# Optimization experiments

Measured on AMD Instinct MI355X. Metric: run time of the kernel, lower is better.

Reference implementation:

```python
import jax, jax.numpy as jnp
import numpy as np

ALPHAS = [2.0 ** k for k in range(-3, 2)]  # cfg.model.mmd.alphas = 2.0
EPS = 1e-12


def _center(x):
    return x - x.mean(axis=-1, keepdims=True)


def _l2norm(x):
    return x / jnp.sqrt(jnp.sum(x * x, axis=-1, keepdims=True) + EPS)


def _multi_gauss(d2):
    # sum_a exp(-a * d2), fused over the alpha list
    out = jnp.exp(-ALPHAS[0] * d2)
    for a in ALPHAS[1:]:
        out = out + jnp.exp(-a * d2)
    return out


def _sq_dists_self(x):
    # x: [..., n, c] -> squared euclidean pairwise [..., n, n]
    sq = jnp.sum(x * x, axis=-1)  # [..., n]
    gram = jnp.einsum('...ic,...jc->...ij', x, x)
    d2 = sq[..., :, None] + sq[..., None, :] - 2.0 * gram
    return jnp.maximum(d2, 0.0)


def setup_inputs() -> dict:
    key = jax.random.key(0)
    k1, k2 = jax.random.split(key)
    support_xf = jax.random.normal(k1, (16, 5, 130, 640), dtype=jnp.float32)
    query_xf = jax.random.normal(k2, (16, 75, 25, 640), dtype=jnp.float32)
    return {"support_xf": support_xf, "query_xf": query_xf}


def reference(support_xf, query_xf):
    # support_xf: [b, n_way, ns, c], query_xf: [b, q, nq, c]
    b, n_way, ns, c = support_xf.shape
    _, q, nq, _ = query_xf.shape

    # centering over feature dim, then l2 norm (cfg.model.mmd.l2norm = True)
    s = _l2norm(_center(support_xf))
    t = _l2norm(_center(query_xf))

    # self Gram kernels
    k_ss = _multi_gauss(_sq_dists_self(s))  # [b, n_way, ns, ns]
    k_qq = _multi_gauss(_sq_dists_self(t))  # [b, q, nq, nq]

    # cross kernel: broadcast instead of materializing expanded 5D copies
    sn = jnp.sum(s * s, axis=-1)  # [b, n_way, ns]
    tn = jnp.sum(t * t, axis=-1)  # [b, q, nq]
    gram_qs = jnp.einsum('bwsc,bqtc->bqwst', s, t)  # [b, q, n_way, ns, nq]
    d2_qs = jnp.maximum(
        sn[:, None, :, :, None] + tn[:, :, None, None, :] - 2.0 * gram_qs, 0.0)
    k_qs = _multi_gauss(d2_qs)

    # MMD terms: unbiased self terms drop the diagonal
    mmd_s = (jnp.sum(k_ss, axis=(-1, -2)) - jnp.trace(k_ss, axis1=-2, axis2=-1)) \
        / (ns * (ns - 1))  # [b, n_way]
    mmd_q = (jnp.sum(k_qq, axis=(-1, -2)) - jnp.trace(k_qq, axis1=-2, axis2=-1)) \
        / (nq * (nq - 1))  # [b, q]
    mmd_qs = jnp.sum(k_qs, axis=(-1, -2)) / (ns * nq)  # [b, q, n_way]

    mmd_dis = mmd_s[:, None, :] + mmd_q[:, :, None] - 2.0 * mmd_qs  # [b, q, n_way]
    return mmd_dis
```

## Files before the change

### kernel.cpp

```cpp
#include <hip/hip_runtime.h>
#include <math.h>


#define EXP_C (-0.25f * 1.44269504088896340736f)

typedef __attribute__((ext_vector_type(8))) short bf16x8_t;
typedef __attribute__((ext_vector_type(4))) float f32x4_t;
typedef unsigned short u16;

#define GLOAD_LDS16(g, l)                                 \
  __builtin_amdgcn_global_load_lds(                       \
      (const __attribute__((address_space(1))) void*)(g), \
      (__attribute__((address_space(3))) void*)(l), 16, 0, 0)

__device__ __forceinline__ u16 f2bf(float f) {
  unsigned int u = __float_as_uint(f);
  unsigned int r = (u + 0x7fffu + ((u >> 16) & 1u)) >> 16;
  return (u16)r;
}

__device__ __forceinline__ float mgauss(float g) {
  float h = fmaxf(1.f - g, 0.f);
  float e1 = exp2f(h * EXP_C);
  float e2 = e1 * e1, e4 = e2 * e2, e8 = e4 * e4, e16 = e8 * e8;
  return e1 + e2 + e4 + e8 + e16;
}

__device__ __forceinline__ float wred(float v) {
#pragma unroll
  for (int m = 1; m < 64; m <<= 1) v += __shfl_xor(v, m, 64);
  return v;
}

__global__ void prep_kernel(const float* __restrict__ S,
                            const float* __restrict__ Q,
                            u16* __restrict__ SHL, u16* __restrict__ QHL,
                            float* __restrict__ accz) {
  int bid = blockIdx.x, tid = threadIdx.x;
  if (bid < 29) {
    int z = bid * 256 + tid;
    if (z < 7280) accz[z] = 0.f;
  }
  int wid = (bid << 2) | (tid >> 6);
  int lane = tid & 63;
  const float* src;
  u16* dst;
  if (wid < 10400) {
    src = S + (size_t)wid * 640;
    dst = SHL + (size_t)wid * 640;
  } else {
    int w2 = wid - 10400;
    src = Q + (size_t)w2 * 640;
    dst = QHL + (size_t)w2 * 640;
  }
  const float4* s4 = (const float4*)src;
  float4 a = s4[lane];
  float4 b = s4[lane + 64];
  float4 c = make_float4(0.f, 0.f, 0.f, 0.f);
  if (lane < 32) c = s4[lane + 128];
  float s = a.x + a.y + a.z + a.w + b.x + b.y + b.z + b.w + c.x + c.y + c.z +
            c.w;
  float ss = a.x * a.x + a.y * a.y + a.z * a.z + a.w * a.w + b.x * b.x +
             b.y * b.y + b.z * b.z + b.w * b.w + c.x * c.x + c.y * c.y +
             c.z * c.z + c.w * c.w;
#pragma unroll
  for (int m = 1; m < 64; m <<= 1) {
    s += __shfl_xor(s, m, 64);
    ss += __shfl_xor(ss, m, 64);
  }
  float mean = s * (1.f / 640.f);
  float inv = 1.f / sqrtf(fmaxf(ss - s * s * (1.f / 640.f), 0.f) + 1e-12f);
  ushort4* d4 = (ushort4*)dst;
  d4[lane] = make_ushort4(f2bf((a.x - mean) * inv), f2bf((a.y - mean) * inv),
                          f2bf((a.z - mean) * inv), f2bf((a.w - mean) * inv));
  d4[lane + 64] =
      make_ushort4(f2bf((b.x - mean) * inv), f2bf((b.y - mean) * inv),
                   f2bf((b.z - mean) * inv), f2bf((b.w - mean) * inv));
  if (lane < 32)
    d4[lane + 128] =
        make_ushort4(f2bf((c.x - mean) * inv), f2bf((c.y - mean) * inv),
                     f2bf((c.z - mean) * inv), f2bf((c.w - mean) * inv));
}

__global__ __launch_bounds__(256, 4) void grams_kernel(
    const u16* __restrict__ SHL, const u16* __restrict__ QHL,
    float* __restrict__ accS, float* __restrict__ accQ,
    float* __restrict__ accQS) {
  __shared__ __align__(16) u16 sA[128 * 64];
  __shared__ __align__(16) u16 sB[128 * 64];
  const int bid = blockIdx.x;
  const int id = (bid & 7) * 242 + (bid >> 3);
  const int tid = threadIdx.x;
  const int w = tid >> 6, l = tid & 63;

  int mode, gb, i0, j0, nx, ny;
  const u16 *pX, *pY;
  if (id < 1440) {
    mode = 0;
    gb = id / 90;
    int r = id % 90;
    i0 = (r % 6) * 128;
    j0 = (r / 6) * 128;
    pX = SHL + (size_t)gb * 650 * 640;
    pY = QHL + (size_t)gb * 1875 * 640;
    nx = 650;
    ny = 1875;
  } else if (id < 1696) {
    mode = 1;
    int t = id - 1440;
    gb = t >> 4;
    int p = t & 15;
    int ti, tj;
    if (p < 4) {
      ti = p >> 1;
      tj = p & 1;
    } else {
      int q = (p - 4) / 3, r3 = (p - 4) % 3;
      ti = (r3 == 0) ? q + 1 : q + 2;
      tj = (r3 == 1) ? q + 1 : q + 2;
    }
    i0 = ti * 128;
    j0 = tj * 128;
    pX = pY = SHL + (size_t)gb * 650 * 640;
    nx = ny = 650;
  } else {
    mode = 2;
    gb = id - 1696;
    i0 = 0;
    j0 = 0;
    pX = pY = QHL + (size_t)gb * 125 * 640;
    nx = ny = 125;
  }

  int st_r[4], st_c[4];
#pragma unroll
  for (int i = 0; i < 4; ++i) {
    int s = (w * 4 + i) * 64 + l;
    st_r[i] = s >> 3;
    st_c[i] = ((s & 7) ^ (st_r[i] & 7)) * 8;
  }

  f32x4_t av[4][4];
#pragma unroll
  for (int i = 0; i < 4; ++i)
#pragma unroll
    for (int j = 0; j < 4; ++j)
#pragma unroll
      for (int r = 0; r < 4; ++r) av[i][j][r] = 0.f;

  const int wr = w >> 1, wc = w & 1;
  const int R0 = wr * 64, C0 = wc * 64;
  const int lr = l & 15, lk8 = (l >> 4) * 8;

  for (int c = 0; c < 10; ++c) {
    int kb = c * 64;
#pragma unroll
    for (int i = 0; i < 4; ++i) {
      int vi = i0 + st_r[i];
      vi = vi < nx ? vi : nx - 1;
      GLOAD_LDS16(pX + (size_t)vi * 640 + kb + st_c[i], &sA[(w * 4 + i) * 512]);
      int vj = j0 + st_r[i];
      vj = vj < ny ? vj : ny - 1;
      GLOAD_LDS16(pY + (size_t)vj * 640 + kb + st_c[i], &sB[(w * 4 + i) * 512]);
    }
    __syncthreads();
#pragma unroll
    for (int ks = 0; ks < 2; ++ks) {
      bf16x8_t af[4], bfv[4];
      int kk = ks * 32 + lk8;
#pragma unroll
      for (int t = 0; t < 4; ++t) {
        int rr = R0 + t * 16 + lr;
        af[t] = *(const bf16x8_t*)&sA[rr * 64 + (kk ^ ((rr & 7) << 3))];
        int cc = C0 + t * 16 + lr;
        bfv[t] = *(const bf16x8_t*)&sB[cc * 64 + (kk ^ ((cc & 7) << 3))];
      }
#pragma unroll
      for (int i = 0; i < 4; ++i)
#pragma unroll
        for (int j = 0; j < 4; ++j)
          av[i][j] = __builtin_amdgcn_mfma_f32_16x16x32_bf16(af[i], bfv[j],
                                                             av[i][j], 0, 0, 0);
    }
    __syncthreads();
  }

  int gcv[4];
  bool cvv[4];
#pragma unroll
  for (int j = 0; j < 4; ++j) {
    gcv[j] = j0 + C0 + j * 16 + lr;
    cvv[j] = gcv[j] < ny;
  }

  if (mode == 0) {
    const int cbi = (i0 + R0) / 130;
    const int cbj = (j0 + C0) / 25;
    int cjr[4];
#pragma unroll
    for (int j = 0; j < 4; ++j) cjr[j] = gcv[j] / 25 - cbj;
    float ce[2][4] = {{0.f, 0.f, 0.f, 0.f}, {0.f, 0.f, 0.f, 0.f}};
#pragma unroll
    for (int i = 0; i < 4; ++i)
#pragma unroll
      for (int rr = 0; rr < 4; ++rr) {
        int gr = i0 + R0 + i * 16 + (l >> 4) * 4 + rr;
        bool rv = gr < 650;
        bool ra = (gr / 130) == cbi;
#pragma unroll
        for (int j = 0; j < 4; ++j) {
          float kv = mgauss(av[i][j][rr]);
          kv = (rv && cvv[j]) ? kv : 0.f;
          float k0 = ra ? kv : 0.f;
          ce[0][j] += k0;
          ce[1][j] += kv - k0;
        }
      }
#pragma unroll
    for (int a = 0; a < 2; ++a)
#pragma unroll
      for (int bq = 0; bq < 4; ++bq) {
        float t = 0.f;
#pragma unroll
        for (int j = 0; j < 4; ++j) t += (cjr[j] == bq) ? ce[a][j] : 0.f;
        t = wred(t);
        if (l == 0) {
          int ci = cbi + a, cj = cbj + bq;
          if (ci < 5 && cj < 75) atomicAdd(&accQS[gb * 375 + cj * 5 + ci], t);
        }
      }
  } else if (mode == 1) {
    const int cbi = (i0 + R0) / 130;
    int ccv[4];
#pragma unroll
    for (int j = 0; j < 4; ++j) ccv[j] = gcv[j] / 130;
    float ce[2][4] = {{0.f, 0.f, 0.f, 0.f}, {0.f, 0.f, 0.f, 0.f}};
#pragma unroll
    for (int i = 0; i < 4; ++i)
#pragma unroll
      for (int rr = 0; rr < 4; ++rr) {
        int gr = i0 + R0 + i * 16 + (l >> 4) * 4 + rr;
        bool rv = gr < 650;
        int rc = gr / 130;
        bool ra = rc == cbi;
#pragma unroll
        for (int j = 0; j < 4; ++j) {
          float kv = mgauss(av[i][j][rr]);
          bool val = rv && cvv[j] && (ccv[j] == rc) && (gr != gcv[j]);
          kv = val ? kv : 0.f;
          float k0 = ra ? kv : 0.f;
          ce[0][j] += k0;
          ce[1][j] += kv - k0;
        }
      }
#pragma unroll
    for (int a = 0; a < 2; ++a) {
      float t = wred(ce[a][0] + ce[a][1] + ce[a][2] + ce[a][3]);
      if (l == 0) {
        int ci = cbi + a;
        if (ci < 5) atomicAdd(&accS[gb * 5 + ci], t);
      }
    }
  } else {
    const int cbi = R0 / 25;
    int ccv[4];
#pragma unroll
    for (int j = 0; j < 4; ++j) ccv[j] = gcv[j] / 25;
    float ce[4][4] = {{0.f, 0.f, 0.f, 0.f},
                      {0.f, 0.f, 0.f, 0.f},
                      {0.f, 0.f, 0.f, 0.f},
                      {0.f, 0.f, 0.f, 0.f}};
#pragma unroll
    for (int i = 0; i < 4; ++i)
#pragma unroll
      for (int rr = 0; rr < 4; ++rr) {
        int gr = R0 + i * 16 + (l >> 4) * 4 + rr;
        bool rv = gr < 125;
        int rc = gr / 25;
        int ar = rc - cbi;
#pragma unroll
        for (int j = 0; j < 4; ++j) {
          float kv = mgauss(av[i][j][rr]);
          bool val = rv && cvv[j] && (ccv[j] == rc) && (gr != gcv[j]);
          kv = val ? kv : 0.f;
#pragma unroll
          for (int a = 0; a < 4; ++a) ce[a][j] += (ar == a) ? kv : 0.f;
        }
      }
#pragma unroll
    for (int a = 0; a < 4; ++a) {
      float t = wred(ce[a][0] + ce[a][1] + ce[a][2] + ce[a][3]);
      if (l == 0) {
        int ci = cbi + a;
        if (ci < 5) atomicAdd(&accQ[gb * 5 + ci], t);
      }
    }
  }
}

__global__ void finalize_kernel(const float* __restrict__ accS,
                                const float* __restrict__ accQ,
                                const float* __restrict__ accQS,
                                float* __restrict__ out) {
  int t = blockIdx.x * blockDim.x + threadIdx.x;
  if (t >= 6000) return;
  int w = t % 5;
  int bq = t / 5;
  int b = t / 375;
  out[t] = accS[b * 5 + w] * (1.f / (130.f * 129.f)) +
           accQ[bq] * (1.f / (25.f * 24.f)) - accQS[t] * (2.f / (130.f * 25.f));
}

extern "C" void kernel_launch(void* const* d_in, const int* in_sizes, int n_in,
                              void* d_out, int out_size, void* d_ws,
                              size_t ws_size, hipStream_t stream) {
  const float* S = (const float*)d_in[0];
  const float* Q = (const float*)d_in[1];
  float* ws = (float*)d_ws;
  float* accS = ws + 0;
  float* accQ = ws + 80;
  float* accQS = ws + 1280;
  u16* SHL = (u16*)(ws + 7280);
  u16* QHL = SHL + (size_t)10400 * 640;
  float* out = (float*)d_out;

  prep_kernel<<<10100, 256, 0, stream>>>(S, Q, SHL, QHL, ws);
  grams_kernel<<<1936, 256, 0, stream>>>(SHL, QHL, accS, accQ, accQS);
  finalize_kernel<<<24, 256, 0, stream>>>(accS, accQ, accQS, out);
}
```

Before: 238.2 us.

## Double-buffer LDS tiles to overlap global loads with MFMA compute

Splits the shared-memory tiles into two buffers and prefetches the next K-chunk via global_load_lds while the current chunk is consumed by MFMA. This removes one barrier per iteration and hides global load latency behind compute. Per-row global pointers are also hoisted out of the loop. LDS use doubles to 64KB per block and launch bounds drop to 2 blocks per CU, which lowers occupancy.

```diff
diff --git a/kernel.cpp b/kernel.cpp
--- a/kernel.cpp
+++ b/kernel.cpp
@@ -82,12 +82,12 @@
                      f2bf((c.z - mean) * inv), f2bf((c.w - mean) * inv));
 }
 
-__global__ __launch_bounds__(256, 4) void grams_kernel(
+__global__ __launch_bounds__(256, 2) void grams_kernel(
     const u16* __restrict__ SHL, const u16* __restrict__ QHL,
     float* __restrict__ accS, float* __restrict__ accQ,
     float* __restrict__ accQS) {
-  __shared__ __align__(16) u16 sA[128 * 64];
-  __shared__ __align__(16) u16 sB[128 * 64];
+  __shared__ __align__(16) u16 sA[2][128 * 64];
+  __shared__ __align__(16) u16 sB[2][128 * 64];
   const int bid = blockIdx.x;
   const int id = (bid & 7) * 242 + (bid >> 3);
   const int tid = threadIdx.x;
@@ -132,12 +132,19 @@
     nx = ny = 125;
   }
 
-  int st_r[4], st_c[4];
+  const u16* gA[4];
+  const u16* gB[4];
 #pragma unroll
   for (int i = 0; i < 4; ++i) {
     int s = (w * 4 + i) * 64 + l;
-    st_r[i] = s >> 3;
-    st_c[i] = ((s & 7) ^ (st_r[i] & 7)) * 8;
+    int r = s >> 3;
+    int c16 = ((s & 7) ^ (r & 7)) * 8;
+    int vi = i0 + r;
+    vi = vi < nx ? vi : nx - 1;
+    gA[i] = pX + (size_t)vi * 640 + c16;
+    int vj = j0 + r;
+    vj = vj < ny ? vj : ny - 1;
+    gB[i] = pY + (size_t)vj * 640 + c16;
   }
 
   f32x4_t av[4][4];
@@ -152,38 +159,42 @@
   const int R0 = wr * 64, C0 = wc * 64;
   const int lr = l & 15, lk8 = (l >> 4) * 8;
 
+#define STAGE(bb, c)                                          \
+  {                                                           \
+    int kb = (c) * 64;                                        \
+    _Pragma("unroll") for (int i = 0; i < 4; ++i) {           \
+      GLOAD_LDS16(gA[i] + kb, &sA[bb][(w * 4 + i) * 512]);    \
+      GLOAD_LDS16(gB[i] + kb, &sB[bb][(w * 4 + i) * 512]);    \
+    }                                                         \
+  }
+
+#define COMPUTE(bb)                                                           \
+  {                                                                           \
+    _Pragma("unroll") for (int ks = 0; ks < 2; ++ks) {                        \
+      bf16x8_t af[4], bfv[4];                                                 \
+      int kk = ks * 32 + lk8;                                                 \
+      _Pragma("unroll") for (int t = 0; t < 4; ++t) {                         \
+        int rr = R0 + t * 16 + lr;                                            \
+        af[t] = *(const bf16x8_t*)&sA[bb][rr * 64 + (kk ^ ((rr & 7) << 3))];  \
+        int cc = C0 + t * 16 + lr;                                            \
+        bfv[t] = *(const bf16x8_t*)&sB[bb][cc * 64 + (kk ^ ((cc & 7) << 3))]; \
+      }                                                                       \
+      _Pragma("unroll") for (int i = 0; i < 4; ++i)                           \
+          _Pragma("unroll") for (int j = 0; j < 4; ++j) av[i][j] =            \
+          __builtin_amdgcn_mfma_f32_16x16x32_bf16(af[i], bfv[j], av[i][j], 0, \
+                                                  0, 0);                      \
+    }                                                                         \
+  }
+
+  STAGE(0, 0);
+  __syncthreads();
   for (int c = 0; c < 10; ++c) {
-    int kb = c * 64;
-#pragma unroll
-    for (int i = 0; i < 4; ++i) {
-      int vi = i0 + st_r[i];
-      vi = vi < nx ? vi : nx - 1;
-      GLOAD_LDS16(pX + (size_t)vi * 640 + kb + st_c[i], &sA[(w * 4 + i) * 512]);
-      int vj = j0 + st_r[i];
-      vj = vj < ny ? vj : ny - 1;
-      GLOAD_LDS16(pY + (size_t)vj * 640 + kb + st_c[i], &sB[(w * 4 + i) * 512]);
-    }
+    if (c < 9) STAGE((c + 1) & 1, c + 1);
+    COMPUTE(c & 1);
     __syncthreads();
-#pragma unroll
-    for (int ks = 0; ks < 2; ++ks) {
-      bf16x8_t af[4], bfv[4];
-      int kk = ks * 32 + lk8;
-#pragma unroll
-      for (int t = 0; t < 4; ++t) {
-        int rr = R0 + t * 16 + lr;
-        af[t] = *(const bf16x8_t*)&sA[rr * 64 + (kk ^ ((rr & 7) << 3))];
-        int cc = C0 + t * 16 + lr;
-        bfv[t] = *(const bf16x8_t*)&sB[cc * 64 + (kk ^ ((cc & 7) << 3))];
-      }
-#pragma unroll
-      for (int i = 0; i < 4; ++i)
-#pragma unroll
-        for (int j = 0; j < 4; ++j)
-          av[i][j] = __builtin_amdgcn_mfma_f32_16x16x32_bf16(af[i], bfv[j],
-                                                             av[i][j], 0, 0, 0);
-    }
-    __syncthreads();
-  }
+  }
+#undef STAGE
+#undef COMPUTE
 
   int gcv[4];
   bool cvv[4];
```

Measured after the change: 216.0 us. 1.1x faster.
